# Kernel tuning notes

Measured on AMD Instinct MI355X. Metric: run time of the kernel, lower is better.

The kernel has to match this reference:

```python
import jax, jax.numpy as jnp
import numpy as np
import math

B, S, D = 2, 2048, 3072
H, KVH = 24, 8
HD = D // H  # 128
N_REP = H // KVH  # 3


def setup_inputs() -> dict:
    key = jax.random.key(0)
    ks = jax.random.split(key, 8)
    x = jax.random.normal(ks[0], (B, S, D), dtype=jnp.float32)
    # RoPE frequencies: cos/sin of theta-scaled angles (real/imag of freqs_cis)
    theta = 500000.0
    inv_freq = 1.0 / (theta ** (np.arange(0, HD, 2, dtype=np.float32) / HD))  # (HD/2,)
    t = np.arange(S, dtype=np.float32)
    ang = np.outer(t, inv_freq)  # (S, HD/2)
    freqs_cos = jnp.asarray(np.cos(ang), dtype=jnp.float32)
    freqs_sin = jnp.asarray(np.sin(ang), dtype=jnp.float32)
    # additive causal mask (1,1,S,S)
    mask = jnp.where(jnp.tril(jnp.ones((S, S), dtype=bool)), 0.0, -1e9).astype(jnp.float32)[None, None]
    scale = 0.02
    wq = jax.random.normal(ks[1], (H * HD, D), dtype=jnp.float32) * scale
    wk = jax.random.normal(ks[2], (KVH * HD, D), dtype=jnp.float32) * scale
    wv = jax.random.normal(ks[3], (KVH * HD, D), dtype=jnp.float32) * scale
    wo = jax.random.normal(ks[4], (D, H * HD), dtype=jnp.float32) * scale
    return {"x": x, "freqs_cos": freqs_cos, "freqs_sin": freqs_sin, "mask": mask,
            "wq": wq, "wk": wk, "wv": wv, "wo": wo}


def _rotate_half(t):
    h = t.shape[-1] // 2
    return jnp.concatenate([-t[..., h:], t[..., :h]], axis=-1)


def reference(x, freqs_cos, freqs_sin, mask, wq, wk, wv, wo):
    b, s, _ = x.shape
    xq = (x @ wq.T).reshape(b, s, H, HD)
    xk = (x @ wk.T).reshape(b, s, KVH, HD)
    xv = (x @ wv.T).reshape(b, s, KVH, HD)
    # RoPE: cos/sin duplicated along last dim, broadcast over batch & heads
    cos = jnp.concatenate([freqs_cos, freqs_cos], axis=-1)[None, :, None, :]  # (1,S,1,HD)
    sin = jnp.concatenate([freqs_sin, freqs_sin], axis=-1)[None, :, None, :]
    xq = xq * cos + _rotate_half(xq) * sin
    xk = xk * cos + _rotate_half(xk) * sin
    # GQA: repeat_interleave KV heads (k0,k0,k0,k1,...) matches jnp.repeat
    keys = jnp.repeat(xk, N_REP, axis=2)    # (B,S,H,HD)
    values = jnp.repeat(xv, N_REP, axis=2)
    scores = jnp.einsum('bqhd,bkhd->bhqk', xq, keys) / math.sqrt(HD)
    scores = scores + mask
    attn = jax.nn.softmax(scores.astype(jnp.float32), axis=-1).astype(xq.dtype)
    out = jnp.einsum('bhqk,bkhd->bqhd', attn, values).reshape(b, s, H * HD)
    return out @ wo.T
```

## Files before the change

### kernel.cpp

```cpp
#include <hip/hip_runtime.h>

typedef unsigned short u16;
typedef unsigned int u32;
typedef __attribute__((ext_vector_type(8))) __bf16 bf16x8;
typedef __attribute__((ext_vector_type(4))) float f32x4;
typedef __attribute__((ext_vector_type(4))) u32 u32x4;
typedef __attribute__((ext_vector_type(8))) u16 u16x8;
typedef __attribute__((ext_vector_type(4))) u16 u16x4;

#define S_LEN 2048
#define DM 3072
#define NH 24
#define NKV 8

__device__ __forceinline__ u16 f2b(float f) {
  u32 u = __builtin_bit_cast(u32, f);
  u = u + 0x7FFFu + ((u >> 16) & 1u);
  return (u16)(u >> 16);
}
__device__ __forceinline__ float b2f(u16 h) {
  u32 u = ((u32)h) << 16;
  return __builtin_bit_cast(float, u);
}
__device__ __forceinline__ f32x4 mfma16(bf16x8 a, bf16x8 b, f32x4 c) {
  return __builtin_amdgcn_mfma_f32_16x16x32_bf16(a, b, c, 0, 0, 0);
}
__device__ __forceinline__ void gload16(const u16* g, u16* l) {
  __builtin_amdgcn_global_load_lds((const __attribute__((address_space(1))) void*)g,
                                   (__attribute__((address_space(3))) void*)l, 16, 0, 0);
}

__device__ __forceinline__ void cvt_one(const float* __restrict__ s, u16* __restrict__ d, int j) {
  const f32x4* p = (const f32x4*)(s + (size_t)j * 8);
  f32x4 a = p[0], b = p[1];
  u16x8 o;
#pragma unroll
  for (int q = 0; q < 4; ++q) { o[q] = f2b(a[q]); o[q + 4] = f2b(b[q]); }
  *(u16x8*)(d + (size_t)j * 8) = o;
}
__global__ __launch_bounds__(256) void cvt4_kernel(const float* __restrict__ s0, u16* __restrict__ d0,
                                                   const float* __restrict__ s1, u16* __restrict__ d1,
                                                   const float* __restrict__ s2, u16* __restrict__ d2,
                                                   const float* __restrict__ s3, u16* __restrict__ d3) {
  int i = blockIdx.x * 256 + threadIdx.x;
  if (i < 1572864)      cvt_one(s0, d0, i);
  else if (i < 2752512) cvt_one(s1, d1, i - 1572864);
  else if (i < 3145728) cvt_one(s2, d2, i - 2752512);
  else                  cvt_one(s3, d3, i - 3145728);
}

__device__ __forceinline__ void swz_bid(int& bx, int& by) {
  int gx = gridDim.x;
  int tot = gx * gridDim.y;
  int id = blockIdx.y * gx + blockIdx.x;
  int cpx = tot >> 3;
  int s = (id & 7) * cpx + (id >> 3);
  bx = s % gx;
  by = s / gx;
}

template <int BN>
__device__ __forceinline__ void gemm256_body(u16* __restrict__ lds,
                                             const u16* __restrict__ A, const u16* __restrict__ B,
                                             void* __restrict__ Cv, int N, int K,
                                             int m0, int n0, int mode,
                                             void* __restrict__ C2 = nullptr,
                                             void* __restrict__ C3 = nullptr) {
  constexpr int NJ = BN / 64;
  constexpr int NSB = BN / 64;
  constexpr int BBUF = NSB * 4096;
  const int tid = threadIdx.x;
  const int lane = tid & 63;
  const int w = tid >> 6;
  const int l15 = lane & 15, g = lane >> 4;
  const int wm = w >> 2, wn = w & 3;
  const int srow = tid >> 3;
  const int scol = ((tid & 7) ^ (srow & 7)) * 8;
  const u16* aS = A + (size_t)(m0 + srow) * K + scol;
  const u16* bS = B + (size_t)(n0 + srow) * K + scol;
  const int sdst = (tid & 448) * 8;
  const int swz0 = (g ^ (l15 & 7)) * 8;
  const int swz1 = ((4 + g) ^ (l15 & 7)) * 8;
  const int aB0 = wm * 8192 + l15 * 64;
  const int bB0 = wn * (BN / 4) * 64 + l15 * 64;

  f32x4 acc[8][NJ];
#pragma unroll
  for (int i = 0; i < 8; ++i)
#pragma unroll
    for (int j = 0; j < NJ; ++j) acc[i][j] = 0.f;

  auto stage = [&](int k0, int bsel) {
#pragma unroll
    for (int s = 0; s < 4; ++s)
      gload16(aS + (size_t)(s * 64) * K + k0, lds + bsel * 16384 + s * 4096 + sdst);
#pragma unroll
    for (int s = 0; s < NSB; ++s)
      gload16(bS + (size_t)(s * 64) * K + k0, lds + 32768 + bsel * BBUF + s * 4096 + sdst);
  };

  stage(0, 0);
  asm volatile("s_waitcnt vmcnt(0)" ::: "memory");
  __builtin_amdgcn_s_barrier();

  for (int t = 0; t < 48; ++t) {
    const int bsel = t & 1;
    const u16* ldsA = lds + bsel * 16384 + aB0;
    const u16* ldsB = lds + 32768 + bsel * BBUF + bB0;
    bf16x8 af[4], bf[NJ];
#pragma unroll
    for (int i = 0; i < 4; ++i) af[i] = *(const bf16x8*)(ldsA + i * 1024 + swz0);
#pragma unroll
    for (int j = 0; j < NJ; ++j) bf[j] = *(const bf16x8*)(ldsB + j * 1024 + swz0);
    if (t < 47) stage((t + 1) * 64, bsel ^ 1);
    asm volatile("" ::: "memory");
    __builtin_amdgcn_s_barrier();
    asm volatile("s_waitcnt lgkmcnt(0)" ::: "memory");
    __builtin_amdgcn_sched_barrier(0);
    __builtin_amdgcn_s_setprio(1);
#pragma unroll
    for (int i = 0; i < 4; ++i)
#pragma unroll
      for (int j = 0; j < NJ; ++j) acc[i][j] = mfma16(af[i], bf[j], acc[i][j]);
    __builtin_amdgcn_s_setprio(0);
    asm volatile("" ::: "memory");
    __builtin_amdgcn_s_barrier();
#pragma unroll
    for (int i = 0; i < 4; ++i) af[i] = *(const bf16x8*)(ldsA + (4 + i) * 1024 + swz0);
    asm volatile("" ::: "memory");
    __builtin_amdgcn_s_barrier();
    asm volatile("s_waitcnt lgkmcnt(0)" ::: "memory");
    __builtin_amdgcn_sched_barrier(0);
    __builtin_amdgcn_s_setprio(1);
#pragma unroll
    for (int i = 0; i < 4; ++i)
#pragma unroll
      for (int j = 0; j < NJ; ++j) acc[4 + i][j] = mfma16(af[i], bf[j], acc[4 + i][j]);
    __builtin_amdgcn_s_setprio(0);
    asm volatile("" ::: "memory");
    __builtin_amdgcn_s_barrier();
#pragma unroll
    for (int i = 0; i < 4; ++i) af[i] = *(const bf16x8*)(ldsA + i * 1024 + swz1);
#pragma unroll
    for (int j = 0; j < NJ; ++j) bf[j] = *(const bf16x8*)(ldsB + j * 1024 + swz1);
    asm volatile("" ::: "memory");
    __builtin_amdgcn_s_barrier();
    asm volatile("s_waitcnt lgkmcnt(0)" ::: "memory");
    __builtin_amdgcn_sched_barrier(0);
    __builtin_amdgcn_s_setprio(1);
#pragma unroll
    for (int i = 0; i < 4; ++i)
#pragma unroll
      for (int j = 0; j < NJ; ++j) acc[i][j] = mfma16(af[i], bf[j], acc[i][j]);
    __builtin_amdgcn_s_setprio(0);
    asm volatile("" ::: "memory");
    __builtin_amdgcn_s_barrier();
#pragma unroll
    for (int i = 0; i < 4; ++i) af[i] = *(const bf16x8*)(ldsA + (4 + i) * 1024 + swz1);
    asm volatile("" ::: "memory");
    asm volatile("s_waitcnt vmcnt(0)" ::: "memory");
    __builtin_amdgcn_s_barrier();
    asm volatile("s_waitcnt lgkmcnt(0)" ::: "memory");
    __builtin_amdgcn_sched_barrier(0);
    __builtin_amdgcn_s_setprio(1);
#pragma unroll
    for (int i = 0; i < 4; ++i)
#pragma unroll
      for (int j = 0; j < NJ; ++j) acc[4 + i][j] = mfma16(af[i], bf[j], acc[4 + i][j]);
    __builtin_amdgcn_s_setprio(0);
    asm volatile("" ::: "memory");
    __builtin_amdgcn_s_barrier();
  }
#pragma unroll
  for (int i = 0; i < 8; ++i)
#pragma unroll
    for (int j = 0; j < NJ; ++j) {
      int nn = n0 + wn * (BN / 4) + j * 16 + l15;
      int mmb = m0 + wm * 128 + i * 16 + g * 4;
      if (mode == 1) {
#pragma unroll
        for (int r = 0; r < 4; ++r)
          ((float*)Cv)[(size_t)(mmb + r) * N + nn] = acc[i][j][r];
      } else if (mode == 0) {
#pragma unroll
        for (int r = 0; r < 4; ++r)
          ((u16*)Cv)[(size_t)(mmb + r) * N + nn] = f2b(acc[i][j][r]);
      } else if (mode == 2) {
        u16x4 pk;
#pragma unroll
        for (int r = 0; r < 4; ++r) pk[r] = f2b(acc[i][j][r]);
        *(u16x4*)((u16*)Cv + (size_t)nn * 2048 + (size_t)(mmb >> 11) * 2097152 + (mmb & 2047)) = pk;
      } else {
        if (nn < 3072) {
#pragma unroll
          for (int r = 0; r < 4; ++r)
            ((u16*)Cv)[(size_t)(mmb + r) * 3072 + nn] = f2b(acc[i][j][r]);
        } else if (nn < 4096) {
#pragma unroll
          for (int r = 0; r < 4; ++r)
            ((u16*)C2)[(size_t)(mmb + r) * 1024 + (nn - 3072)] = f2b(acc[i][j][r]);
        } else {
          int d = nn - 4096;
          u16x4 pk;
#pragma unroll
          for (int r = 0; r < 4; ++r) pk[r] = f2b(acc[i][j][r]);
          *(u16x4*)((u16*)C3 + (size_t)d * 2048 + (size_t)(mmb >> 11) * 2097152 + (mmb & 2047)) = pk;
        }
      }
    }
}

__global__ __launch_bounds__(512, 1) void gemm_qkv(const u16* __restrict__ A,
                                                   const u16* __restrict__ Wcat,
                                                   u16* __restrict__ Cq,
                                                   u16* __restrict__ Ck, u16* __restrict__ Cv,
                                                   int K) {
  __shared__ __align__(16) u16 lds[73728];
  int id = blockIdx.x;
  int s = (id & 7) * 32 + (id >> 3);
  int by = s >> 4, c = s & 15;
  gemm256_body<320>(lds, A, Wcat, Cq, 0, K, by * 256, c * 320, 3, Ck, Cv);
}
__global__ __launch_bounds__(512, 1) void gemm192_f32(const u16* __restrict__ A, const u16* __restrict__ B,
                                                      float* __restrict__ C, int N, int K) {
  __shared__ __align__(16) u16 lds[57344];
  int bx, by; swz_bid(bx, by);
  gemm256_body<192>(lds, A, B, C, N, K, by * 256, bx * 192, 1);
}

__global__ __launch_bounds__(256) void rope_kernel(u16* __restrict__ t, const float* __restrict__ fc,
                                                   const float* __restrict__ fs, int nheads, int total) {
  int idx = blockIdx.x * 256 + threadIdx.x;
  if (idx >= total) return;
  int c = idx & 7;
  int tmp = idx >> 3;
  int h = tmp % nheads;
  int row = tmp / nheads;
  int s = row & (S_LEN - 1);
  int d0 = c << 3;
  u16* base = t + (size_t)row * (nheads * 128) + h * 128;
  u16x8 lo = *(const u16x8*)(base + d0);
  u16x8 hi = *(const u16x8*)(base + 64 + d0);
  const float* cp = fc + s * 64 + d0;
  const float* sp = fs + s * 64 + d0;
  u16x8 olo, ohi;
#pragma unroll
  for (int j = 0; j < 8; ++j) {
    float cv = cp[j], sn = sp[j];
    float a = b2f(lo[j]), b = b2f(hi[j]);
    olo[j] = f2b(a * cv - b * sn);
    ohi[j] = f2b(b * cv + a * sn);
  }
  *(u16x8*)(base + d0) = olo;
  *(u16x8*)(base + 64 + d0) = ohi;
}

__global__ __launch_bounds__(256, 2) void attn_kernel(const u16* __restrict__ xq,
                                                      const u16* __restrict__ xk,
                                                      const u16* __restrict__ xvT,
                                                      const float* __restrict__ fc,
                                                      const float* __restrict__ fs,
                                                      u16* __restrict__ o,
                                                      const float* __restrict__ wo,
                                                      u16* __restrict__ wob) {
  __shared__ __align__(16) u16 smem[40960];
  if (blockIdx.x >= 768) {
    int i = (blockIdx.x - 768) * 256 + threadIdx.x;
    cvt_one(wo, wob, i);
    return;
  }
  const int tid = threadIdx.x;
  const int w = tid >> 6, lane = tid & 63;
  const int l15 = lane & 15, g = lane >> 4;
  const int id = blockIdx.x;
  const int xcd = id & 7, slot = id >> 3;
  const int grp = xcd + 8 * (slot / 48);
  const int s48 = slot % 48;
  const int b = grp >> 3, kvh = grp & 7;
  const int qb = 15 - s48 / 3;
  const int h = kvh * 3 + s48 % 3;
  const float sc2 = 0.08838834764831845f * 1.4426950408889634f;

  const u16* ksrc = xk + (size_t)b * 2097152 + kvh * 128;
  const u16* vsrc = xvT + (size_t)(b * 1024 + kvh * 128) * 2048;
  int koff[4], vofs[4], dst4[4];
#pragma unroll
  for (int r = 0; r < 4; ++r) {
    int c = r * 256 + tid;
    int krow = c >> 4, kj = (c & 15) ^ (krow & 7);
    koff[r] = krow * 1024 + kj * 8;
    int vrow = c >> 3, vj = (c & 7) ^ (vrow & 7);
    vofs[r] = vrow * 2048 + vj * 8;
    dst4[r] = (r * 256 + (tid & 192)) * 8;
  }
  u16* sPw = smem + 32768 + w * 2048;
  const int pxr = (l15 & 7) << 3;

  const int q0 = qb * 128;

  bf16x8 qf[2][4];
#pragma unroll
  for (int s = 0; s < 2; ++s) {
    const int qrow = q0 + w * 32 + s * 16 + l15;
    const u16* qptr = xq + (size_t)(b * S_LEN + qrow) * DM + h * 128;
#pragma unroll
    for (int dcp = 0; dcp < 2; ++dcp) {
      u16x8 Lo = *(const u16x8*)(qptr + dcp * 32 + g * 8);
      u16x8 Hi = *(const u16x8*)(qptr + 64 + dcp * 32 + g * 8);
      const float* cp = fc + qrow * 64 + dcp * 32 + g * 8;
      const float* sp = fs + qrow * 64 + dcp * 32 + g * 8;
      bf16x8 qlo, qhi;
#pragma unroll
      for (int j = 0; j < 8; ++j) {
        float cv = cp[j], sn = sp[j];
        float a = b2f(Lo[j]), bb = b2f(Hi[j]);
        qlo[j] = (__bf16)((a * cv - bb * sn) * sc2);
        qhi[j] = (__bf16)((bb * cv + a * sn) * sc2);
      }
      qf[s][dcp] = qlo;
      qf[s][dcp + 2] = qhi;
    }
  }

  u16 *sKc = smem, *sKn = smem + 8192;
  u16 *sVc = smem + 16384, *sVn = smem + 24576;

  f32x4 accO[2][8];
#pragma unroll
  for (int s = 0; s < 2; ++s)
#pragma unroll
    for (int i = 0; i < 8; ++i) accO[s][i] = 0.f;
  float m_[2] = {-1e30f, -1e30f}, ls_[2] = {0.f, 0.f};
  const int nt = 2 * qb + 2;

#pragma unroll
  for (int r = 0; r < 4; ++r) gload16(ksrc + koff[r], sKc + dst4[r]);
#pragma unroll
  for (int r = 0; r < 4; ++r) gload16(vsrc + vofs[r], sVc + dst4[r]);
  __syncthreads();

  for (int t = 0; t < nt; ++t) {
    if (t + 1 < nt) {
      int k0n = (t + 1) * 64;
#pragma unroll
      for (int r = 0; r < 4; ++r) gload16(ksrc + (size_t)k0n * 1024 + koff[r], sKn + dst4[r]);
#pragma unroll
      for (int r = 0; r < 4; ++r) gload16(vsrc + k0n + vofs[r], sVn + dst4[r]);
    }
    if (64 * t <= q0 + w * 32 + 31) {
      f32x4 st[2][4];
      __builtin_amdgcn_s_setprio(1);
#pragma unroll
      for (int kt = 0; kt < 4; ++kt) {
        int row = kt * 16 + l15;
        bf16x8 kf[4];
#pragma unroll
        for (int dc = 0; dc < 4; ++dc)
          kf[dc] = *(const bf16x8*)(sKc + row * 128 + ((dc * 32 + g * 8) ^ ((row & 7) << 3)));
        f32x4 a0 = 0.f, a1 = 0.f;
#pragma unroll
        for (int dc = 0; dc < 4; ++dc) {
          a0 = mfma16(kf[dc], qf[0][dc], a0);
          a1 = mfma16(kf[dc], qf[1][dc], a1);
        }
        st[0][kt] = a0;
        st[1][kt] = a1;
      }
      __builtin_amdgcn_s_setprio(0);
#pragma unroll
      for (int s = 0; s < 2; ++s) {
        const int qrow = q0 + w * 32 + s * 16 + l15;
        float pmax = -1e30f;
#pragma unroll
        for (int kt = 0; kt < 4; ++kt)
#pragma unroll
          for (int r = 0; r < 4; ++r) {
            float x = st[s][kt][r];
            if (t >= nt - 2) {
              int kk = t * 64 + kt * 16 + g * 4 + r;
              if (kk > qrow) x = -1e30f;
            }
            st[s][kt][r] = x;
            pmax = fmaxf(pmax, x);
          }
        pmax = fmaxf(pmax, __shfl_xor(pmax, 16));
        pmax = fmaxf(pmax, __shfl_xor(pmax, 32));
        if (!__all(pmax - m_[s] <= 8.0f)) {
          float mnew = fmaxf(m_[s], pmax);
          float corr = exp2f(m_[s] - mnew);
          ls_[s] *= corr;
#pragma unroll
          for (int i = 0; i < 8; ++i) accO[s][i] *= corr;
          m_[s] = mnew;
        }
        float ps = 0.f;
#pragma unroll
        for (int kt = 0; kt < 4; ++kt) {
          u16x4 pk;
#pragma unroll
          for (int r = 0; r < 4; ++r) {
            float p = exp2f(st[s][kt][r] - m_[s]);
            ps += p;
            pk[r] = f2b(p);
          }
          *(u16x4*)(sPw + s * 1024 + ((l15 * 64 + kt * 16 + g * 4) ^ pxr)) = pk;
        }
        ps += __shfl_xor(ps, 16);
        ps += __shfl_xor(ps, 32);
        ls_[s] += ps;
      }
      bf16x8 pf[2][2];
#pragma unroll
      for (int s = 0; s < 2; ++s)
#pragma unroll
        for (int ck = 0; ck < 2; ++ck)
          pf[s][ck] = *(const bf16x8*)(sPw + s * 1024 + ((l15 * 64 + ck * 32 + g * 8) ^ pxr));
      __builtin_amdgcn_s_setprio(1);
#pragma unroll
      for (int dt = 0; dt < 8; ++dt) {
        int row = dt * 16 + l15;
#pragma unroll
        for (int ck = 0; ck < 2; ++ck) {
          bf16x8 vf = *(const bf16x8*)(sVc + row * 64 + ((ck * 32 + g * 8) ^ ((row & 7) << 3)));
          accO[0][dt] = mfma16(vf, pf[0][ck], accO[0][dt]);
          accO[1][dt] = mfma16(vf, pf[1][ck], accO[1][dt]);
        }
      }
      __builtin_amdgcn_s_setprio(0);
    }
    __syncthreads();
    u16* tk = sKc; sKc = sKn; sKn = tk;
    u16* tv = sVc; sVc = sVn; sVn = tv;
  }
  u16* sOw = smem + w * 8192;
#pragma unroll
  for (int s = 0; s < 2; ++s) {
    float invl = 1.0f / ls_[s];
#pragma unroll
    for (int dt = 0; dt < 8; ++dt)
#pragma unroll
      for (int r = 0; r < 4; ++r) {
        int d = dt * 16 + g * 4 + r;
        sOw[((s * 16 + l15) * 128 + d) ^ pxr] = f2b(accO[s][dt][r] * invl);
      }
  }
#pragma unroll
  for (int p = 0; p < 8; ++p) {
    int idx = p * 64 + lane;
    int q = idx >> 4, c = idx & 15;
    int j = c ^ (q & 7);
    u32x4 v = *(const u32x4*)(sOw + q * 128 + j * 8);
    *(u32x4*)(o + (size_t)(b * S_LEN + q0 + w * 32 + q) * DM + h * 128 + c * 8) = v;
  }
}

extern "C" void kernel_launch(void* const* d_in, const int* in_sizes, int n_in,
                              void* d_out, int out_size, void* d_ws, size_t ws_size,
                              hipStream_t stream) {
  const float* x  = (const float*)d_in[0];
  const float* fc = (const float*)d_in[1];
  const float* fs = (const float*)d_in[2];
  const float* wq = (const float*)d_in[4];
  const float* wk = (const float*)d_in[5];
  const float* wv = (const float*)d_in[6];
  const float* wo = (const float*)d_in[7];
  float* out = (float*)d_out;
  char* ws = (char*)d_ws;

  u16* xb  = (u16*)(ws);
  u16* wqb = (u16*)(ws + 25165824);
  u16* att = (u16*)(ws + 25165824);
  u16* wkb = (u16*)(ws + 44040192);
  u16* wvb = (u16*)(ws + 50331648);
  u16* xqb = (u16*)(ws + 56623104);
  u16* xkb = (u16*)(ws + 81788928);
  u16* xvT = (u16*)(ws + 90177536);
  u16* wob = (u16*)(ws);

  cvt4_kernel<<<13824, 256, 0, stream>>>(x, xb, wq, wqb, wk, wkb, wv, wvb);

  gemm_qkv<<<256, 512, 0, stream>>>(xb, wqb, xqb, xkb, xvT, 3072);

  rope_kernel<<<1024, 256, 0, stream>>>(xkb, fc, fs, NKV, 4096 * NKV * 8);

  attn_kernel<<<5376, 256, 0, stream>>>(xqb, xkb, xvT, fc, fs, att, wo, wob);

  gemm192_f32<<<dim3(16, 16), 512, 0, stream>>>(att, wob, out, 3072, 3072);
}
```

Before: 328.6 us.

## Split B staging across phases with partial vmcnt waits in GEMM mainloop

Restructures the GEMM main loop so the next tile's B sub-blocks are issued in pieces across the four compute phases, and waits use partial vmcnt counts instead of a full drain. It also changes the N mapping: each warp now owns interleaved 16-column slices across 64-column sub-blocks. This lets each phase load only the B fragments it needs, with all 8 A fragments loaded at once. The aim is to overlap global-to-LDS traffic with MFMA work and avoid stalling on every outstanding load. The cost is higher register pressure from holding 8 A fragments, and the hand-tuned wait counts must stay correct for each NJ.

```diff
diff --git a/kernel.cpp b/kernel.cpp
--- a/kernel.cpp
+++ b/kernel.cpp
@@ -12,6 +12,8 @@
 #define DM 3072
 #define NH 24
 #define NKV 8
+
+#define WAITV(n) asm volatile("s_waitcnt vmcnt(" #n ")" ::: "memory")
 
 __device__ __forceinline__ u16 f2b(float f) {
   u32 u = __builtin_bit_cast(u32, f);
@@ -67,8 +69,7 @@
                                              void* __restrict__ C2 = nullptr,
                                              void* __restrict__ C3 = nullptr) {
   constexpr int NJ = BN / 64;
-  constexpr int NSB = BN / 64;
-  constexpr int BBUF = NSB * 4096;
+  constexpr int BBUF = NJ * 4096;
   const int tid = threadIdx.x;
   const int lane = tid & 63;
   const int w = tid >> 6;
@@ -82,7 +83,7 @@
   const int swz0 = (g ^ (l15 & 7)) * 8;
   const int swz1 = ((4 + g) ^ (l15 & 7)) * 8;
   const int aB0 = wm * 8192 + l15 * 64;
-  const int bB0 = wn * (BN / 4) * 64 + l15 * 64;
+  const int bB0 = wn * 1024 + l15 * 64;
 
   f32x4 acc[8][NJ];
 #pragma unroll
@@ -90,83 +91,95 @@
 #pragma unroll
     for (int j = 0; j < NJ; ++j) acc[i][j] = 0.f;
 
-  auto stage = [&](int k0, int bsel) {
+  auto stgA = [&](int k0, int bsel) {
 #pragma unroll
     for (int s = 0; s < 4; ++s)
       gload16(aS + (size_t)(s * 64) * K + k0, lds + bsel * 16384 + s * 4096 + sdst);
-#pragma unroll
-    for (int s = 0; s < NSB; ++s)
-      gload16(bS + (size_t)(s * 64) * K + k0, lds + 32768 + bsel * BBUF + s * 4096 + sdst);
   };
-
-  stage(0, 0);
-  asm volatile("s_waitcnt vmcnt(0)" ::: "memory");
+  auto stgB = [&](int k0, int bsel, int s) {
+    gload16(bS + (size_t)(s * 64) * K + k0, lds + 32768 + bsel * BBUF + s * 4096 + sdst);
+  };
+
+  stgA(0, 0);
+#pragma unroll
+  for (int s = 0; s < NJ; ++s) stgB(0, 0, s);
+  if constexpr (NJ == 5) WAITV(3); else WAITV(1);
   __builtin_amdgcn_s_barrier();
 
   for (int t = 0; t < 48; ++t) {
-    const int bsel = t & 1;
+    const int bsel = t & 1, nsel = bsel ^ 1;
+    const int kn = (t + 1) * 64;
+    const bool st = (t < 47);
     const u16* ldsA = lds + bsel * 16384 + aB0;
     const u16* ldsB = lds + 32768 + bsel * BBUF + bB0;
-    bf16x8 af[4], bf[NJ];
-#pragma unroll
-    for (int i = 0; i < 4; ++i) af[i] = *(const bf16x8*)(ldsA + i * 1024 + swz0);
-#pragma unroll
-    for (int j = 0; j < NJ; ++j) bf[j] = *(const bf16x8*)(ldsB + j * 1024 + swz0);
-    if (t < 47) stage((t + 1) * 64, bsel ^ 1);
-    asm volatile("" ::: "memory");
+    bf16x8 af[8], b0, b1, bx[NJ - 2];
+#pragma unroll
+    for (int mi = 0; mi < 8; ++mi) af[mi] = *(const bf16x8*)(ldsA + mi * 1024 + swz0);
+    b0 = *(const bf16x8*)(ldsB + swz0);
+    b1 = *(const bf16x8*)(ldsB + 4096 + swz0);
+    if (st) stgA(kn, nsel);
+    asm volatile("" ::: "memory");
+    if (st) WAITV(4); else WAITV(0);
     __builtin_amdgcn_s_barrier();
     asm volatile("s_waitcnt lgkmcnt(0)" ::: "memory");
     __builtin_amdgcn_sched_barrier(0);
     __builtin_amdgcn_s_setprio(1);
 #pragma unroll
-    for (int i = 0; i < 4; ++i)
-#pragma unroll
-      for (int j = 0; j < NJ; ++j) acc[i][j] = mfma16(af[i], bf[j], acc[i][j]);
+    for (int mi = 0; mi < 8; ++mi) {
+      acc[mi][0] = mfma16(af[mi], b0, acc[mi][0]);
+      acc[mi][1] = mfma16(af[mi], b1, acc[mi][1]);
+    }
     __builtin_amdgcn_s_setprio(0);
     asm volatile("" ::: "memory");
     __builtin_amdgcn_s_barrier();
 #pragma unroll
-    for (int i = 0; i < 4; ++i) af[i] = *(const bf16x8*)(ldsA + (4 + i) * 1024 + swz0);
+    for (int j = 2; j < NJ; ++j) bx[j - 2] = *(const bf16x8*)(ldsB + j * 4096 + swz0);
+    if (st) { stgB(kn, nsel, 0); stgB(kn, nsel, 1); }
     asm volatile("" ::: "memory");
     __builtin_amdgcn_s_barrier();
     asm volatile("s_waitcnt lgkmcnt(0)" ::: "memory");
     __builtin_amdgcn_sched_barrier(0);
     __builtin_amdgcn_s_setprio(1);
 #pragma unroll
-    for (int i = 0; i < 4; ++i)
-#pragma unroll
-      for (int j = 0; j < NJ; ++j) acc[4 + i][j] = mfma16(af[i], bf[j], acc[4 + i][j]);
+    for (int mi = 0; mi < 8; ++mi)
+#pragma unroll
+      for (int j = 2; j < NJ; ++j) acc[mi][j] = mfma16(af[mi], bx[j - 2], acc[mi][j]);
     __builtin_amdgcn_s_setprio(0);
     asm volatile("" ::: "memory");
     __builtin_amdgcn_s_barrier();
 #pragma unroll
-    for (int i = 0; i < 4; ++i) af[i] = *(const bf16x8*)(ldsA + i * 1024 + swz1);
-#pragma unroll
-    for (int j = 0; j < NJ; ++j) bf[j] = *(const bf16x8*)(ldsB + j * 1024 + swz1);
+    for (int mi = 0; mi < 8; ++mi) af[mi] = *(const bf16x8*)(ldsA + mi * 1024 + swz1);
+    b0 = *(const bf16x8*)(ldsB + swz1);
+    b1 = *(const bf16x8*)(ldsB + 4096 + swz1);
+    if (st) { stgB(kn, nsel, 2); if constexpr (NJ == 5) stgB(kn, nsel, 3); }
     asm volatile("" ::: "memory");
     __builtin_amdgcn_s_barrier();
     asm volatile("s_waitcnt lgkmcnt(0)" ::: "memory");
     __builtin_amdgcn_sched_barrier(0);
     __builtin_amdgcn_s_setprio(1);
 #pragma unroll
-    for (int i = 0; i < 4; ++i)
-#pragma unroll
-      for (int j = 0; j < NJ; ++j) acc[i][j] = mfma16(af[i], bf[j], acc[i][j]);
+    for (int mi = 0; mi < 8; ++mi) {
+      acc[mi][0] = mfma16(af[mi], b0, acc[mi][0]);
+      acc[mi][1] = mfma16(af[mi], b1, acc[mi][1]);
+    }
     __builtin_amdgcn_s_setprio(0);
     asm volatile("" ::: "memory");
     __builtin_amdgcn_s_barrier();
 #pragma unroll
-    for (int i = 0; i < 4; ++i) af[i] = *(const bf16x8*)(ldsA + (4 + i) * 1024 + swz1);
-    asm volatile("" ::: "memory");
-    asm volatile("s_waitcnt vmcnt(0)" ::: "memory");
+    for (int j = 2; j < NJ; ++j) bx[j - 2] = *(const bf16x8*)(ldsB + j * 4096 + swz1);
+    if (st) {
+      if constexpr (NJ == 5) stgB(kn, nsel, 4);
+      asm volatile("" ::: "memory");
+      if constexpr (NJ == 5) WAITV(3); else WAITV(1);
+    }
     __builtin_amdgcn_s_barrier();
     asm volatile("s_waitcnt lgkmcnt(0)" ::: "memory");
     __builtin_amdgcn_sched_barrier(0);
     __builtin_amdgcn_s_setprio(1);
 #pragma unroll
-    for (int i = 0; i < 4; ++i)
-#pragma unroll
-      for (int j = 0; j < NJ; ++j) acc[4 + i][j] = mfma16(af[i], bf[j], acc[4 + i][j]);
+    for (int mi = 0; mi < 8; ++mi)
+#pragma unroll
+      for (int j = 2; j < NJ; ++j) acc[mi][j] = mfma16(af[mi], bx[j - 2], acc[mi][j]);
     __builtin_amdgcn_s_setprio(0);
     asm volatile("" ::: "memory");
     __builtin_amdgcn_s_barrier();
@@ -175,7 +188,7 @@
   for (int i = 0; i < 8; ++i)
 #pragma unroll
     for (int j = 0; j < NJ; ++j) {
-      int nn = n0 + wn * (BN / 4) + j * 16 + l15;
+      int nn = n0 + j * 64 + wn * 16 + l15;
       int mmb = m0 + wm * 128 + i * 16 + g * 4;
       if (mode == 1) {
 #pragma unroll
```

After: 313.5 us. 4.6% less time.
